# Kernel optimization log

Hardware: AMD Instinct MI355X
Metric: run time of the kernel (lower is better)

Reference implementation:

```python
import jax, jax.numpy as jnp
import numpy as np

N, E = 100000, 1600000
F_IN, F_HID, F_OUT = 64, 64, 16


def setup_inputs() -> dict:
    key = jax.random.key(0)
    ks = jax.random.split(key, 10)
    def g(k, shape):
        return jax.random.normal(k, shape, dtype=jnp.float32) * 0.05
    return {
        "x": jax.random.normal(ks[0], (N, F_IN), dtype=jnp.float32),
        "adj": jax.random.randint(ks[1], (2, E), 0, N, dtype=jnp.int32),
        # ChebConv K=2 params: per-order weights [in, out] + shared bias
        "W1_0": g(ks[2], (F_IN, F_HID)), "W1_1": g(ks[3], (F_IN, F_HID)),
        "b1": jnp.zeros((F_HID,), jnp.float32),
        "Wx_0": g(ks[4], (F_HID, F_HID)), "Wx_1": g(ks[5], (F_HID, F_HID)),
        "bx": jnp.zeros((F_HID,), jnp.float32),
        "W2_0": g(ks[6], (F_HID, F_OUT)), "W2_1": g(ks[7], (F_HID, F_OUT)),
        "b2": jnp.zeros((F_OUT,), jnp.float32),
    }


def _cheb(x, row, col, w, W0, W1, b):
    # K=2 Chebyshev conv: Tx0 = x, Tx1 = L_hat @ x (sparse propagate)
    n = x.shape[0]
    tx1 = jax.ops.segment_sum(w[:, None] * x[col], row, num_segments=n)
    return x @ W0 + tx1 @ W1 + b


def reference(x, adj, W1_0, W1_1, b1, Wx_0, Wx_1, bx, W2_0, W2_1, b2):
    row, col = adj[0], adj[1]
    n = x.shape[0]
    # sym-normalized Laplacian scaled by 2/lambda_max (=1): diagonal cancels,
    # off-diagonal weight = -deg^{-1/2}[row] * deg^{-1/2}[col]
    deg = jax.ops.segment_sum(jnp.ones(adj.shape[1], x.dtype), row, num_segments=n)
    dis = jnp.where(deg > 0, jax.lax.rsqrt(jnp.maximum(deg, 1e-12)), 0.0)
    w = -dis[row] * dis[col]
    h = jax.nn.relu(_cheb(x, row, col, w, W1_0, W1_1, b1))
    # dropout is identity in eval mode
    h = jax.nn.relu(_cheb(h, row, col, w, Wx_0, Wx_1, bx))
    return _cheb(h, row, col, w, W2_0, W2_1, b2)
```

## Files before the change

kernel.cpp:

```cpp
#include <hip/hip_runtime.h>
#include <hip/hip_bf16.h>


#define EPB 4096

typedef __attribute__((ext_vector_type(8))) short bf16x8;
typedef __attribute__((ext_vector_type(4))) float f32x4;

__device__ __forceinline__ float bf2f(unsigned short u) {
    unsigned int x = ((unsigned int)u) << 16;
    return __uint_as_float(x);
}
__device__ __forceinline__ unsigned short f2bf(float f) {
    unsigned int b = __float_as_uint(f);
    unsigned int r = (b + 0x7FFF + ((b >> 16) & 1)) >> 16;
    return (unsigned short)r;
}
__device__ __forceinline__ void acc8(float* a, bf16x8 v) {
#pragma unroll
    for (int i = 0; i < 8; ++i) a[i] += bf2f((unsigned short)(short)v[i]);
}

template <int NC>
__device__ __forceinline__ void pack_pair(const float* __restrict__ W0,
                                          const float* __restrict__ W1,
                                          unsigned short* __restrict__ out, int idx) {
    constexpr int NT = NC / 16;
    int i = idx & 7;
    int m = (idx >> 3) & 15;
    int g = (idx >> 7) & 3;
    int f = idx >> 9;
    int nt = f % NT;
    int kt = f / NT;
    const float* W = (kt < 2) ? W0 : W1;
    int k = (kt & 1) * 32 + g * 8 + i;
    out[idx] = f2bf(W[k * NC + nt * 16 + m]);
}

__global__ __launch_bounds__(256) void wconv_all(const float* __restrict__ W1_0,
                                                 const float* __restrict__ W1_1,
                                                 const float* __restrict__ Wx_0,
                                                 const float* __restrict__ Wx_1,
                                                 const float* __restrict__ W2_0,
                                                 const float* __restrict__ W2_1,
                                                 unsigned short* __restrict__ wp1,
                                                 unsigned short* __restrict__ wpx,
                                                 unsigned short* __restrict__ wp2,
                                                 int* __restrict__ bcnt, int nbk) {
    int idx = blockIdx.x * 256 + threadIdx.x;
    if (idx < nbk) bcnt[idx] = 0;
    if (idx < 8192) pack_pair<64>(W1_0, W1_1, wp1, idx);
    else if (idx < 16384) pack_pair<64>(Wx_0, Wx_1, wpx, idx - 8192);
    else if (idx < 18432) pack_pair<16>(W2_0, W2_1, wp2, idx - 16384);
}

__global__ __launch_bounds__(256) void bucket_count(const int* __restrict__ row,
                                                    int* __restrict__ bcnt,
                                                    int e, int nbk) {
    __shared__ int bh[512];
    int tid = threadIdx.x;
    for (int j = tid; j < nbk; j += 256) bh[j] = 0;
    __syncthreads();
    int base = blockIdx.x * EPB;
#pragma unroll
    for (int k = 0; k < EPB / 256; ++k) {
        int i = base + k * 256 + tid;
        if (i < e) atomicAdd(&bh[row[i] >> 8], 1);
    }
    __syncthreads();
    for (int j = tid; j < nbk; j += 256) {
        int c = bh[j];
        if (c) atomicAdd(&bcnt[j], c);
    }
}

__global__ __launch_bounds__(256) void bucket_scan(const int* __restrict__ bcnt,
                                                   int* __restrict__ bbase,
                                                   int* __restrict__ bcursor,
                                                   int* __restrict__ off,
                                                   int nbk, int n, int e) {
    __shared__ int sa[512], sb[512];
    int tid = threadIdx.x;
    for (int j = tid; j < 512; j += 256) sa[j] = (j < nbk) ? bcnt[j] : 0;
    __syncthreads();
    int* in = sa;
    int* out = sb;
    for (int d = 1; d < 512; d <<= 1) {
        for (int j = tid; j < 512; j += 256)
            out[j] = in[j] + ((j >= d) ? in[j - d] : 0);
        __syncthreads();
        int* t = in; in = out; out = t;
    }
    for (int j = tid; j < nbk; j += 256) {
        int incl = in[j];
        int excl = incl - bcnt[j];
        bbase[j] = excl;
        bcursor[j] = excl;
        if (j == nbk - 1) bbase[nbk] = incl;
    }
    if (tid == 0) off[n] = e;
}

__global__ __launch_bounds__(256) void bucket_scatter(const int* __restrict__ row,
                                                      const int* __restrict__ col,
                                                      int* __restrict__ bcursor,
                                                      int* __restrict__ packed,
                                                      int e, int nbk) {
    __shared__ int bh[512];
    __shared__ int bbase[512];
    __shared__ int bcur[512];
    int tid = threadIdx.x;
    for (int j = tid; j < nbk; j += 256) { bh[j] = 0; bcur[j] = 0; }
    __syncthreads();
    int base = blockIdx.x * EPB;
#pragma unroll
    for (int k = 0; k < EPB / 256; ++k) {
        int i = base + k * 256 + tid;
        if (i < e) atomicAdd(&bh[row[i] >> 8], 1);
    }
    __syncthreads();
    for (int j = tid; j < nbk; j += 256) {
        int c = bh[j];
        bbase[j] = c ? atomicAdd(&bcursor[j], c) : 0;
    }
    __syncthreads();
#pragma unroll
    for (int k = 0; k < EPB / 256; ++k) {
        int i = base + k * 256 + tid;
        if (i < e) {
            int r = row[i];
            int b = r >> 8;
            int slot = bbase[b] + atomicAdd(&bcur[b], 1);
            packed[slot] = ((r & 255) << 17) | col[i];
        }
    }
}

__global__ __launch_bounds__(256) void bucket_build(const int* __restrict__ packed,
                                                    const int* __restrict__ bbase,
                                                    const float* __restrict__ x,
                                                    int* __restrict__ off,
                                                    float* __restrict__ dis,
                                                    int* __restrict__ csr,
                                                    unsigned short* __restrict__ y,
                                                    unsigned short* __restrict__ xb,
                                                    int n) {
    __shared__ int rcnt[256];
    __shared__ int sa[256], sb[256];
    __shared__ float disv[256];
    int tid = threadIdx.x;
    int b = blockIdx.x;
    int ebase = bbase[b], eend = bbase[b + 1];
    rcnt[tid] = 0;
    __syncthreads();
    for (int e = ebase + tid; e < eend; e += 256)
        atomicAdd(&rcnt[packed[e] >> 17], 1);
    __syncthreads();
    sa[tid] = rcnt[tid];
    __syncthreads();
    int* in = sa;
    int* out = sb;
    for (int d = 1; d < 256; d <<= 1) {
        out[tid] = in[tid] + ((tid >= d) ? in[tid - d] : 0);
        __syncthreads();
        int* t = in; in = out; out = t;
    }
    int grow = b * 256 + tid;
    int c = rcnt[tid];
    int excl = in[tid] - c;
    float dv = (c > 0) ? rsqrtf((float)c) : 0.0f;
    disv[tid] = dv;
    if (grow < n) {
        off[grow] = ebase + excl;
        dis[grow] = dv;
    }
    out[tid] = excl;
    __syncthreads();
    for (int e = ebase + tid; e < eend; e += 256) {
        int p = packed[e];
        int lr = p >> 17;
        int pos = atomicAdd(&out[lr], 1);
        csr[ebase + pos] = p & 0x1FFFF;
    }
    for (int idx = tid; idx < 4096; idx += 256) {
        int rr = idx >> 4, q = idx & 15;
        int R = b * 256 + rr;
        if (R < n) {
            float d = disv[rr];
            float4 v = ((const float4*)x)[(size_t)R * 16 + q];
            ushort4 o = {f2bf(v.x * d), f2bf(v.y * d), f2bf(v.z * d), f2bf(v.w * d)};
            ((ushort4*)y)[(size_t)R * 16 + q] = o;
            ushort4 xo = {f2bf(v.x), f2bf(v.y), f2bf(v.z), f2bf(v.w)};
            ((ushort4*)xb)[(size_t)R * 16 + q] = xo;
        }
    }
}


template <int NC, bool RELU, bool WRITE_HY>
__global__ __launch_bounds__(256) void agg_dense(const unsigned short* __restrict__ y,
                                                 const unsigned short* __restrict__ A0,
                                                 const int* __restrict__ csr,
                                                 const int* __restrict__ off,
                                                 const float* __restrict__ dis,
                                                 const unsigned short* __restrict__ Wp,
                                                 const float* __restrict__ bias,
                                                 unsigned short* __restrict__ hout,
                                                 unsigned short* __restrict__ yout,
                                                 float* __restrict__ fout,
                                                 int n) {
    constexpr int NT = NC / 16;
    __shared__ unsigned short txl[64 * 64];
    int tid = threadIdx.x;

    int row_l = tid >> 2;
    int fq = tid & 3;
    int r = blockIdx.x * 64 + row_l;
    float acc16[16];
#pragma unroll
    for (int i = 0; i < 16; ++i) acc16[i] = 0.f;
    float d = 0.f;
    if (r < n) {
        int s0 = off[r], e1 = off[r + 1];
        const unsigned short* Yb = y + fq * 16;
        int t = s0;
        for (; t + 4 <= e1; t += 4) {
            int c0 = csr[t], c1 = csr[t + 1], c2 = csr[t + 2], c3 = csr[t + 3];
            const bf16x8* p0 = (const bf16x8*)(Yb + (size_t)c0 * 64);
            const bf16x8* p1 = (const bf16x8*)(Yb + (size_t)c1 * 64);
            const bf16x8* p2 = (const bf16x8*)(Yb + (size_t)c2 * 64);
            const bf16x8* p3 = (const bf16x8*)(Yb + (size_t)c3 * 64);
            bf16x8 v00 = p0[0], v01 = p0[1];
            bf16x8 v10 = p1[0], v11 = p1[1];
            bf16x8 v20 = p2[0], v21 = p2[1];
            bf16x8 v30 = p3[0], v31 = p3[1];
            acc8(acc16, v00); acc8(acc16 + 8, v01);
            acc8(acc16, v10); acc8(acc16 + 8, v11);
            acc8(acc16, v20); acc8(acc16 + 8, v21);
            acc8(acc16, v30); acc8(acc16 + 8, v31);
        }
        for (; t < e1; ++t) {
            int c = csr[t];
            const bf16x8* pc = (const bf16x8*)(Yb + (size_t)c * 64);
            bf16x8 v0 = pc[0], v1 = pc[1];
            acc8(acc16, v0); acc8(acc16 + 8, v1);
        }
        d = -dis[r];
    }
    bf16x8 ov0, ov1;
#pragma unroll
    for (int i = 0; i < 8; ++i) {
        ov0[i] = (short)f2bf(acc16[i] * d);
        ov1[i] = (short)f2bf(acc16[8 + i] * d);
    }
    int swz = (row_l & 7) << 4;
    int cb = fq * 32;
    *(bf16x8*)((char*)txl + row_l * 128 + (cb ^ swz)) = ov0;
    *(bf16x8*)((char*)txl + row_l * 128 + ((cb + 16) ^ swz)) = ov1;
    __syncthreads();

    int lane = tid & 63;
    int m = lane & 15;
    int g = lane >> 4;
    int w = tid >> 6;
    const bf16x8* WP = (const bf16x8*)Wp;
    bf16x8 bf[NT][4];
#pragma unroll
    for (int kt = 0; kt < 4; ++kt)
#pragma unroll
        for (int nt = 0; nt < NT; ++nt)
            bf[nt][kt] = WP[((kt * NT + nt) * 4 + g) * 16 + m];
    int r0 = blockIdx.x * 64 + w * 16;
    int ra = r0 + m;
    if (ra > n - 1) ra = n - 1;
    const unsigned short* q0 = A0 + (size_t)ra * 64 + g * 8;
    bf16x8 a0 = *(const bf16x8*)q0;
    bf16x8 a1 = *(const bf16x8*)(q0 + 32);
    int rl2 = w * 16 + m;
    int sw2 = (m & 7) << 4;
    bf16x8 a2 = *(bf16x8*)((char*)txl + rl2 * 128 + ((g * 16) ^ sw2));
    bf16x8 a3 = *(bf16x8*)((char*)txl + rl2 * 128 + ((64 + g * 16) ^ sw2));
    f32x4 acc[NT];
#pragma unroll
    for (int nt = 0; nt < NT; ++nt) {
        float b = bias[nt * 16 + m];
        acc[nt][0] = b; acc[nt][1] = b; acc[nt][2] = b; acc[nt][3] = b;
    }
#pragma unroll
    for (int nt = 0; nt < NT; ++nt) {
        acc[nt] = __builtin_amdgcn_mfma_f32_16x16x32_bf16(a0, bf[nt][0], acc[nt], 0, 0, 0);
        acc[nt] = __builtin_amdgcn_mfma_f32_16x16x32_bf16(a1, bf[nt][1], acc[nt], 0, 0, 0);
        acc[nt] = __builtin_amdgcn_mfma_f32_16x16x32_bf16(a2, bf[nt][2], acc[nt], 0, 0, 0);
        acc[nt] = __builtin_amdgcn_mfma_f32_16x16x32_bf16(a3, bf[nt][3], acc[nt], 0, 0, 0);
    }
#pragma unroll
    for (int reg = 0; reg < 4; ++reg) {
        int rr = r0 + 4 * g + reg;
        if (rr >= n) continue;
        if (WRITE_HY) {
            float dv = dis[rr];
#pragma unroll
            for (int nt = 0; nt < NT; ++nt) {
                float v = acc[nt][reg];
                if (RELU) v = fmaxf(v, 0.f);
                hout[(size_t)rr * NC + nt * 16 + m] = f2bf(v);
                yout[(size_t)rr * NC + nt * 16 + m] = f2bf(v * dv);
            }
        } else {
#pragma unroll
            for (int nt = 0; nt < NT; ++nt)
                fout[(size_t)rr * NC + nt * 16 + m] = acc[nt][reg];
        }
    }
}


extern "C" void kernel_launch(void* const* d_in, const int* in_sizes, int n_in,
                              void* d_out, int out_size, void* d_ws, size_t ws_size,
                              hipStream_t stream) {
    const float* x    = (const float*)d_in[0];
    const int*   adj  = (const int*)d_in[1];
    const float* W1_0 = (const float*)d_in[2];
    const float* W1_1 = (const float*)d_in[3];
    const float* b1   = (const float*)d_in[4];
    const float* Wx_0 = (const float*)d_in[5];
    const float* Wx_1 = (const float*)d_in[6];
    const float* bx   = (const float*)d_in[7];
    const float* W2_0 = (const float*)d_in[8];
    const float* W2_1 = (const float*)d_in[9];
    const float* b2   = (const float*)d_in[10];
    float* out = (float*)d_out;

    int N = in_sizes[0] / 64;
    int E = in_sizes[1] / 2;
    const int* row = adj;
    const int* col = adj + E;
    int NBK = (N + 255) / 256;

    char* p = (char*)d_ws;
    auto alloc = [&](size_t bytes) {
        char* q = p;
        p += (bytes + 255) & ~(size_t)255;
        return q;
    };
    int*   bcnt  = (int*)alloc((size_t)(NBK) * 4);
    int*   bbase = (int*)alloc((size_t)(NBK + 1) * 4);
    int*   bcur  = (int*)alloc((size_t)(NBK) * 4);
    int*   off   = (int*)alloc((size_t)(N + 1) * 4);
    float* dis   = (float*)alloc((size_t)N * 4);
    int*   csr   = (int*)alloc((size_t)E * 4);
    int*   packed = (int*)alloc((size_t)E * 4);
    unsigned short* wp1 = (unsigned short*)alloc(8192 * 2);
    unsigned short* wpx = (unsigned short*)alloc(8192 * 2);
    unsigned short* wp2 = (unsigned short*)alloc(2048 * 2);
    unsigned short* y  = (unsigned short*)alloc((size_t)N * 64 * 2);
    unsigned short* y2 = (unsigned short*)alloc((size_t)N * 64 * 2);
    unsigned short* xb = (unsigned short*)alloc((size_t)N * 64 * 2);
    unsigned short* h  = (unsigned short*)alloc((size_t)N * 64 * 2);
    unsigned short* h2 = (unsigned short*)alloc((size_t)N * 64 * 2);
    (void)ws_size;

    int EB = (E + EPB - 1) / EPB;
    wconv_all<<<72, 256, 0, stream>>>(W1_0, W1_1, Wx_0, Wx_1, W2_0, W2_1,
                                      wp1, wpx, wp2, bcnt, NBK);
    bucket_count<<<EB, 256, 0, stream>>>(row, bcnt, E, NBK);
    bucket_scan<<<1, 256, 0, stream>>>(bcnt, bbase, bcur, off, NBK, N, E);
    bucket_scatter<<<EB, 256, 0, stream>>>(row, col, bcur, packed, E, NBK);
    bucket_build<<<NBK, 256, 0, stream>>>(packed, bbase, x, off, dis, csr, y, xb, N);

    int nb64 = (N + 63) / 64;
    agg_dense<64, true, true><<<nb64, 256, 0, stream>>>(y, xb, csr, off, dis, wp1, b1, h, y2, nullptr, N);
    agg_dense<64, true, true><<<nb64, 256, 0, stream>>>(y2, h, csr, off, dis, wpx, bx, h2, y, nullptr, N);
    agg_dense<16, false, false><<<nb64, 256, 0, stream>>>(y, h2, csr, off, dis, wp2, b2, nullptr, nullptr, out, N);
}
```

Measured before the change: 188.3 us.

## Split aggregation rows across 8 threads and halve rows per block

The sparse aggregation now assigns 8 threads per row, each gathering a 16-byte slice, instead of 4 threads each loading 32 bytes. Blocks cover 32 rows, and the MFMA stage splits output columns across wave pairs. The aim is more memory-level parallelism, deeper unrolling (8 neighbors in flight) and more blocks for latency hiding. In exchange, every wave reloads the A operand rows, and in the 16-column layer half of the waves sit idle.

```diff
diff --git a/kernel.cpp b/kernel.cpp
--- a/kernel.cpp
+++ b/kernel.cpp
@@ -209,85 +209,81 @@
                                                  unsigned short* __restrict__ yout,
                                                  float* __restrict__ fout,
                                                  int n) {
-    constexpr int NT = NC / 16;
-    __shared__ unsigned short txl[64 * 64];
-    int tid = threadIdx.x;
-
-    int row_l = tid >> 2;
-    int fq = tid & 3;
-    int r = blockIdx.x * 64 + row_l;
-    float acc16[16];
-#pragma unroll
-    for (int i = 0; i < 16; ++i) acc16[i] = 0.f;
+    constexpr int NT2 = (NC == 64) ? 2 : 1;
+    __shared__ unsigned short txl[32 * 64];
+    int tid = threadIdx.x;
+
+    int row_l = tid >> 3;
+    int fo = (tid & 7) * 8;
+    int r = blockIdx.x * 32 + row_l;
+    float a8[8];
+#pragma unroll
+    for (int i = 0; i < 8; ++i) a8[i] = 0.f;
     float d = 0.f;
     if (r < n) {
         int s0 = off[r], e1 = off[r + 1];
-        const unsigned short* Yb = y + fq * 16;
+        const unsigned short* Yb = y + fo;
         int t = s0;
-        for (; t + 4 <= e1; t += 4) {
+        for (; t + 8 <= e1; t += 8) {
             int c0 = csr[t], c1 = csr[t + 1], c2 = csr[t + 2], c3 = csr[t + 3];
-            const bf16x8* p0 = (const bf16x8*)(Yb + (size_t)c0 * 64);
-            const bf16x8* p1 = (const bf16x8*)(Yb + (size_t)c1 * 64);
-            const bf16x8* p2 = (const bf16x8*)(Yb + (size_t)c2 * 64);
-            const bf16x8* p3 = (const bf16x8*)(Yb + (size_t)c3 * 64);
-            bf16x8 v00 = p0[0], v01 = p0[1];
-            bf16x8 v10 = p1[0], v11 = p1[1];
-            bf16x8 v20 = p2[0], v21 = p2[1];
-            bf16x8 v30 = p3[0], v31 = p3[1];
-            acc8(acc16, v00); acc8(acc16 + 8, v01);
-            acc8(acc16, v10); acc8(acc16 + 8, v11);
-            acc8(acc16, v20); acc8(acc16 + 8, v21);
-            acc8(acc16, v30); acc8(acc16 + 8, v31);
+            int c4 = csr[t + 4], c5 = csr[t + 5], c6 = csr[t + 6], c7 = csr[t + 7];
+            bf16x8 v0 = *(const bf16x8*)(Yb + (size_t)c0 * 64);
+            bf16x8 v1 = *(const bf16x8*)(Yb + (size_t)c1 * 64);
+            bf16x8 v2 = *(const bf16x8*)(Yb + (size_t)c2 * 64);
+            bf16x8 v3 = *(const bf16x8*)(Yb + (size_t)c3 * 64);
+            bf16x8 v4 = *(const bf16x8*)(Yb + (size_t)c4 * 64);
+            bf16x8 v5 = *(const bf16x8*)(Yb + (size_t)c5 * 64);
+            bf16x8 v6 = *(const bf16x8*)(Yb + (size_t)c6 * 64);
+            bf16x8 v7 = *(const bf16x8*)(Yb + (size_t)c7 * 64);
+            acc8(a8, v0); acc8(a8, v1); acc8(a8, v2); acc8(a8, v3);
+            acc8(a8, v4); acc8(a8, v5); acc8(a8, v6); acc8(a8, v7);
         }
         for (; t < e1; ++t) {
             int c = csr[t];
-            const bf16x8* pc = (const bf16x8*)(Yb + (size_t)c * 64);
-            bf16x8 v0 = pc[0], v1 = pc[1];
-            acc8(acc16, v0); acc8(acc16 + 8, v1);
+            bf16x8 v = *(const bf16x8*)(Yb + (size_t)c * 64);
+            acc8(a8, v);
         }
         d = -dis[r];
     }
-    bf16x8 ov0, ov1;
-#pragma unroll
-    for (int i = 0; i < 8; ++i) {
-        ov0[i] = (short)f2bf(acc16[i] * d);
-        ov1[i] = (short)f2bf(acc16[8 + i] * d);
-    }
+    bf16x8 ov;
+#pragma unroll
+    for (int i = 0; i < 8; ++i) ov[i] = (short)f2bf(a8[i] * d);
     int swz = (row_l & 7) << 4;
-    int cb = fq * 32;
-    *(bf16x8*)((char*)txl + row_l * 128 + (cb ^ swz)) = ov0;
-    *(bf16x8*)((char*)txl + row_l * 128 + ((cb + 16) ^ swz)) = ov1;
+    *(bf16x8*)((char*)txl + row_l * 128 + ((fo * 2) ^ swz)) = ov;
     __syncthreads();
 
     int lane = tid & 63;
     int m = lane & 15;
     int g = lane >> 4;
     int w = tid >> 6;
+    int t16 = (NC == 64) ? (w >> 1) : w;
+    int ch = (NC == 64) ? (w & 1) : 0;
+    if (NC == 16 && w >= 2) return;
     const bf16x8* WP = (const bf16x8*)Wp;
-    bf16x8 bf[NT][4];
+    bf16x8 bf[NT2][4];
 #pragma unroll
     for (int kt = 0; kt < 4; ++kt)
 #pragma unroll
-        for (int nt = 0; nt < NT; ++nt)
-            bf[nt][kt] = WP[((kt * NT + nt) * 4 + g) * 16 + m];
-    int r0 = blockIdx.x * 64 + w * 16;
+        for (int nt = 0; nt < NT2; ++nt)
+            bf[nt][kt] = WP[((kt * (NC / 16) + ch * NT2 + nt) * 4 + g) * 16 + m];
+    int r0 = blockIdx.x * 32 + t16 * 16;
     int ra = r0 + m;
     if (ra > n - 1) ra = n - 1;
     const unsigned short* q0 = A0 + (size_t)ra * 64 + g * 8;
     bf16x8 a0 = *(const bf16x8*)q0;
     bf16x8 a1 = *(const bf16x8*)(q0 + 32);
-    int rl2 = w * 16 + m;
+    int rl2 = t16 * 16 + m;
     int sw2 = (m & 7) << 4;
     bf16x8 a2 = *(bf16x8*)((char*)txl + rl2 * 128 + ((g * 16) ^ sw2));
     bf16x8 a3 = *(bf16x8*)((char*)txl + rl2 * 128 + ((64 + g * 16) ^ sw2));
-    f32x4 acc[NT];
-#pragma unroll
-    for (int nt = 0; nt < NT; ++nt) {
-        float b = bias[nt * 16 + m];
+    f32x4 acc[NT2];
+#pragma unroll
+    for (int nt = 0; nt < NT2; ++nt) {
+        float b = bias[(ch * NT2 + nt) * 16 + m];
         acc[nt][0] = b; acc[nt][1] = b; acc[nt][2] = b; acc[nt][3] = b;
     }
 #pragma unroll
-    for (int nt = 0; nt < NT; ++nt) {
+    for (int nt = 0; nt < NT2; ++nt) {
         acc[nt] = __builtin_amdgcn_mfma_f32_16x16x32_bf16(a0, bf[nt][0], acc[nt], 0, 0, 0);
         acc[nt] = __builtin_amdgcn_mfma_f32_16x16x32_bf16(a1, bf[nt][1], acc[nt], 0, 0, 0);
         acc[nt] = __builtin_amdgcn_mfma_f32_16x16x32_bf16(a2, bf[nt][2], acc[nt], 0, 0, 0);
@@ -300,16 +296,17 @@
         if (WRITE_HY) {
             float dv = dis[rr];
 #pragma unroll
-            for (int nt = 0; nt < NT; ++nt) {
+            for (int nt = 0; nt < NT2; ++nt) {
+                int cc = (ch * NT2 + nt) * 16 + m;
                 float v = acc[nt][reg];
                 if (RELU) v = fmaxf(v, 0.f);
-                hout[(size_t)rr * NC + nt * 16 + m] = f2bf(v);
-                yout[(size_t)rr * NC + nt * 16 + m] = f2bf(v * dv);
+                hout[(size_t)rr * NC + cc] = f2bf(v);
+                yout[(size_t)rr * NC + cc] = f2bf(v * dv);
             }
         } else {
 #pragma unroll
-            for (int nt = 0; nt < NT; ++nt)
-                fout[(size_t)rr * NC + nt * 16 + m] = acc[nt][reg];
+            for (int nt = 0; nt < NT2; ++nt)
+                fout[(size_t)rr * NC + (ch * NT2 + nt) * 16 + m] = acc[nt][reg];
         }
     }
 }
@@ -368,8 +365,8 @@
     bucket_scatter<<<EB, 256, 0, stream>>>(row, col, bcur, packed, E, NBK);
     bucket_build<<<NBK, 256, 0, stream>>>(packed, bbase, x, off, dis, csr, y, xb, N);
 
-    int nb64 = (N + 63) / 64;
-    agg_dense<64, true, true><<<nb64, 256, 0, stream>>>(y, xb, csr, off, dis, wp1, b1, h, y2, nullptr, N);
-    agg_dense<64, true, true><<<nb64, 256, 0, stream>>>(y2, h, csr, off, dis, wpx, bx, h2, y, nullptr, N);
-    agg_dense<16, false, false><<<nb64, 256, 0, stream>>>(y, h2, csr, off, dis, wp2, b2, nullptr, nullptr, out, N);
-}
+    int nb32 = (N + 31) / 32;
+    agg_dense<64, true, true><<<nb32, 256, 0, stream>>>(y, xb, csr, off, dis, wp1, b1, h, y2, nullptr, N);
+    agg_dense<64, true, true><<<nb32, 256, 0, stream>>>(y2, h, csr, off, dis, wpx, bx, h2, y, nullptr, N);
+    agg_dense<16, false, false><<<nb32, 256, 0, stream>>>(y, h2, csr, off, dis, wp2, b2, nullptr, nullptr, out, N);
+}
```

After: 204.4 us. 8.5% more time.
